# Kernel optimization log

Measured on AMD Instinct MI355X. Metric: run time of the kernel, lower is better.

Reference implementation:

```python
import jax, jax.numpy as jnp
import numpy as np

N = 10000   # num_nodes
E = 320000  # num_edges
D = 256     # feature / hidden dim
H = 256


def adj_lap(edge_index, n):
    """Dense normalized adjacency (gcn_norm, no self loops) and sym Laplacian."""
    row, col = edge_index[0], edge_index[1]
    # dense 0/1 adjacency (duplicate edges overwrite with same value, as in the loop)
    A = jnp.zeros((n, n), dtype=jnp.float32).at[row, col].set(1.0)
    # gcn_norm: deg = scatter(w, col) -> column sums
    deg_c = A.sum(axis=0)
    dinv_c = jnp.where(deg_c > 0, jax.lax.rsqrt(jnp.maximum(deg_c, 1e-12)), 0.0)
    anorm = dinv_c[:, None] * A * dinv_c[None, :]
    # get_laplacian 'sym': deg = scatter(w, row) -> row sums; L = I - D^-1/2 A D^-1/2
    deg_r = A.sum(axis=1)
    dinv_r = jnp.where(deg_r > 0, jax.lax.rsqrt(jnp.maximum(deg_r, 1e-12)), 0.0)
    lap = jnp.eye(n, dtype=jnp.float32) - dinv_r[:, None] * A * dinv_r[None, :]
    return lap, anorm


def gcn2(x, M, W1, b1, W2, b2):
    # pretrain_model: two-layer spectral GCN using propagation matrix M
    h = jax.nn.relu(M @ (x @ W1) + b1)
    return M @ (h @ W2) + b2


def setup_inputs() -> dict:
    key = jax.random.key(0)
    k1, k2, k3, k4 = jax.random.split(key, 4)
    x = jax.random.normal(k1, (N, D), dtype=jnp.float32)
    edge_index = jax.random.randint(k2, (2, E), 0, N, dtype=jnp.int64)
    W1 = jax.random.normal(k3, (D, H), dtype=jnp.float32) * 0.05
    b1 = jnp.zeros((H,), dtype=jnp.float32)
    W2 = jax.random.normal(k4, (H, H), dtype=jnp.float32) * 0.05
    b2 = jnp.zeros((H,), dtype=jnp.float32)
    return {"x": x, "edge_index": edge_index, "W1": W1, "b1": b1, "W2": W2, "b2": b2}


def reference(x, edge_index, W1, b1, W2, b2):
    # identity augmentor: x1 = x2 = x, edge_index1 = edge_index2 = edge_index,
    # so adj_lap is identical for both branches (computed once).
    lsym, anorm = adj_lap(edge_index, x.shape[0])
    z1 = gcn2(x, lsym, W1, b1, W2, b2)   # 'high' pass
    z2 = gcn2(x, anorm, W1, b1, W2, b2)  # 'low' pass
    z = z2
    return (z, z1, z2)
```

## Files before the change

### kernel.cpp

```cpp
#include <hip/hip_runtime.h>

#define NN 10000
#define EE 320000
#define HH 256
#define BKT 192

typedef __attribute__((ext_vector_type(8))) short bf16x8;
typedef __attribute__((ext_vector_type(4))) float f32x4;

__device__ float bf2f(unsigned int v) {
    return __uint_as_float(v << 16);
}
__device__ unsigned short f2bf(float f) {
    unsigned int i = __float_as_uint(f);
    return (unsigned short)((i + 0x7fffu + ((i >> 16) & 1u)) >> 16);
}
__device__ unsigned int fp8e(float f) {
    float a = fabsf(f);
    a = fminf(a, 448.0f);
    unsigned int bits = __float_as_uint(a * __uint_as_float(0x03800000u));
    bits = bits + 0x7ffffu + ((bits >> 20) & 1u);
    unsigned int r = bits >> 20;
    if (r > 0x7eu) r = 0x7eu;
    return r | ((__float_as_uint(f) >> 24) & 0x80u);
}
__device__ float fp8d(unsigned int b) {
    float mag = __uint_as_float((b & 0x7fu) << 20) * __uint_as_float(0x7B800000u);
    return __uint_as_float(((b & 0x80u) << 24) | __float_as_uint(mag));
}
__device__ unsigned int pk2(unsigned short a, unsigned short b) {
    return (unsigned int)a | ((unsigned int)b << 16);
}

__device__ int eload(const void* ei, int is64, int idx) {
    if (is64) return (int)(((const long long*)ei)[idx]);
    return ((const int*)ei)[idx];
}

__global__ void k_init(const unsigned int* xu, const unsigned int* eu, int* flags,
                       int* slotcnt, int* deg_c) {
    int b = blockIdx.x, t = threadIdx.x;
    int i = b * 256 + t;
    if (i < NN) { slotcnt[i] = 0; deg_c[i] = 0; }
    if (b != 0) return;
    __shared__ int odd_nz;
    __shared__ int plaus;
    if (t == 0) { odd_nz = 0; plaus = 0; }
    __syncthreads();
    if (t < 64) {
        for (int k = t; k < 256; k += 64) {
            if (eu[2 * k + 1] != 0) atomicOr(&odd_nz, 1);
        }
        unsigned int lo = xu[t] & 0xffffu;
        unsigned int ex = (lo >> 7) & 0xffu;
        if (lo == 0u || (ex >= 90u && ex <= 150u)) atomicAdd(&plaus, 1);
    }
    __syncthreads();
    if (t == 0) {
        flags[0] = odd_nz ? 0 : 1;
        flags[1] = (plaus >= 56) ? 0 : 1;
    }
}

__global__ void k_prep_scatter(const void* W1, const void* W2, const void* ei,
                               const int* flags, unsigned short* W1sw,
                               unsigned short* W2sw, int* slotcnt,
                               unsigned short* bucket) {
    int b = blockIdx.x;
    if (b >= 64) {
        int e = (b - 64) * 256 + threadIdx.x;
        int is64 = flags[0];
        int r = eload(ei, is64, e);
        int c = eload(ei, is64, EE + e);
        if (r < 0 || r >= NN || c < 0 || c >= NN) return;
        int slot = atomicAdd(&slotcnt[r], 1);
        if (slot < BKT) bucket[(size_t)r * BKT + slot] = (unsigned short)c;
        return;
    }
    const void* W = (b < 32) ? W1 : W2;
    unsigned short* O = (b < 32) ? W1sw : W2sw;
    int g = ((b < 32) ? b : b - 32) * 256 + threadIdx.x;
    int lane = g & 63;
    int n = (g >> 6) & 15;
    int ks = g >> 10;
    int coln = n * 16 + (lane & 15);
    int krow = ks * 32 + ((lane >> 4) & 3) * 8;
    unsigned short v[8];
    if (flags[1]) {
        const float* Wf = (const float*)W;
        #pragma unroll
        for (int j = 0; j < 8; j++) v[j] = f2bf(Wf[(size_t)(krow + j) * HH + coln]);
    } else {
        const unsigned short* Wh = (const unsigned short*)W;
        #pragma unroll
        for (int j = 0; j < 8; j++) v[j] = Wh[(size_t)(krow + j) * HH + coln];
    }
    uint4 p;
    p.x = pk2(v[0], v[1]); p.y = pk2(v[2], v[3]);
    p.z = pk2(v[4], v[5]); p.w = pk2(v[6], v[7]);
    *(uint4*)(O + (size_t)g * 8) = p;
}

__global__ void k_gy_dedup(const void* A, const unsigned short* Bsw,
                           unsigned char* Yf8, void* Oout, const int* flags,
                           const int* slotcnt, unsigned short* bucket,
                           int* deg_r, int* deg_c) {
    __shared__ unsigned short As[16][264];
    __shared__ int lds[4][BKT];
    __shared__ int cnt[4];
    int b = blockIdx.x;
    int tid = threadIdx.x;
    if (b < 625) {
        int r0 = b * 16;
        int af32 = flags[1];
        {
            int row = tid >> 4, seg = tid & 15;
            if (af32) {
                const float* ap = (const float*)A + (size_t)(r0 + row) * HH + seg * 16;
                unsigned short v[16];
                #pragma unroll
                for (int j = 0; j < 16; j += 4) {
                    float4 q = *(const float4*)(ap + j);
                    v[j] = f2bf(q.x); v[j + 1] = f2bf(q.y);
                    v[j + 2] = f2bf(q.z); v[j + 3] = f2bf(q.w);
                }
                uint4 p0, p1;
                p0.x = pk2(v[0], v[1]);  p0.y = pk2(v[2], v[3]);
                p0.z = pk2(v[4], v[5]);  p0.w = pk2(v[6], v[7]);
                p1.x = pk2(v[8], v[9]);  p1.y = pk2(v[10], v[11]);
                p1.z = pk2(v[12], v[13]); p1.w = pk2(v[14], v[15]);
                *(uint4*)&As[row][seg * 16] = p0;
                *(uint4*)&As[row][seg * 16 + 8] = p1;
            } else {
                const unsigned short* ap = (const unsigned short*)A + (size_t)(r0 + row) * HH + seg * 16;
                *(uint4*)&As[row][seg * 16] = *(const uint4*)ap;
                *(uint4*)&As[row][seg * 16 + 8] = *(const uint4*)(ap + 8);
            }
        }
        __syncthreads();
        int wv = tid >> 6;
        int lane = tid & 63;
        int quad = lane >> 4;
        int l16 = lane & 15;
        f32x4 acc[4] = {{0,0,0,0},{0,0,0,0},{0,0,0,0},{0,0,0,0}};
        for (int ks = 0; ks < 8; ks++) {
            bf16x8 af = *(const bf16x8*)&As[l16][ks * 32 + quad * 8];
            #pragma unroll
            for (int t = 0; t < 4; t++) {
                int n = wv * 4 + t;
                bf16x8 bf = *(const bf16x8*)(Bsw + ((size_t)(ks * 16 + n) * 64 + lane) * 8);
                acc[t] = __builtin_amdgcn_mfma_f32_16x16x32_bf16(af, bf, acc[t], 0, 0, 0);
            }
        }
        size_t chunkW = (size_t)NN * HH;
        #pragma unroll
        for (int t = 0; t < 4; t++) {
            int cn = (wv * 4 + t) * 16 + l16;
            #pragma unroll
            for (int r = 0; r < 4; r++) {
                int row = r0 + quad * 4 + r;
                float v = acc[t][r];
                size_t idx = (size_t)row * HH + cn;
                Yf8[idx] = (unsigned char)fp8e(v);
                if (af32) ((float*)Oout)[2 * chunkW + idx] = v;
                else      ((unsigned short*)Oout)[2 * chunkW + idx] = f2bf(v);
            }
        }
        return;
    }
    int wave = tid >> 6;
    int lane = tid & 63;
    int i = (b - 625) * 4 + wave;
    int d = slotcnt[i];
    if (d > BKT) d = BKT;
    if (lane == 0) cnt[wave] = 0;
    unsigned short* bp = bucket + (size_t)i * BKT;
    for (int t = lane; t < d; t += 64) lds[wave][t] = (int)bp[t];
    __syncthreads();
    for (int t = lane; t < d; t += 64) {
        int c = lds[wave][t];
        int dup = 0;
        for (int u = 0; u < t; u++) dup |= (lds[wave][u] == c);
        if (!dup) {
            int p = atomicAdd(&cnt[wave], 1);
            bp[p] = (unsigned short)c;
            atomicAdd(&deg_c[c], 1);
        }
    }
    __syncthreads();
    if (lane == 0) deg_r[i] = cnt[wave];
}

__global__ void k_dinv2(const int* deg_r, const int* deg_c, float* dinv2) {
    int i = blockIdx.x * 256 + threadIdx.x;
    if (i >= NN) return;
    int dr = deg_r[i], dc = deg_c[i];
    dinv2[2 * i]     = dr > 0 ? rsqrtf((float)dr) : 0.0f;
    dinv2[2 * i + 1] = dc > 0 ? rsqrtf((float)dc) : 0.0f;
}

__global__ void k_spmm_mid(const unsigned char* Yf8, const void* Oout,
                           const unsigned short* bucket, const int* ucnt,
                           const float* dinv2, const void* bias,
                           const int* flags, unsigned short* H1, unsigned short* H2) {
    int wave = threadIdx.x >> 6;
    int lane = threadIdx.x & 63;
    int fb = lane * 4;
    int i = blockIdx.x * 4 + wave;
    float a1[4] = {0, 0, 0, 0};
    float a2[4] = {0, 0, 0, 0};
    int n = ucnt[i];
    const unsigned short* cp = bucket + (size_t)i * BKT;
    int t = 0;
    for (; t + 4 <= n; t += 4) {
        ushort4 c4 = *(const ushort4*)(cp + t);
        int cx[4] = {(int)c4.x, (int)c4.y, (int)c4.z, (int)c4.w};
        float2 w[4];
        #pragma unroll
        for (int j = 0; j < 4; j++) w[j] = *(const float2*)(dinv2 + 2 * cx[j]);
        unsigned int gv[4];
        #pragma unroll
        for (int j = 0; j < 4; j++)
            gv[j] = *(const unsigned int*)(Yf8 + (size_t)cx[j] * 256 + fb);
        #pragma unroll
        for (int j = 0; j < 4; j++) {
            #pragma unroll
            for (int k = 0; k < 4; k++) {
                float y = fp8d((gv[j] >> (8 * k)) & 0xffu);
                a1[k] += w[j].x * y;
                a2[k] += w[j].y * y;
            }
        }
    }
    for (; t < n; t++) {
        int c = (int)cp[t];
        float2 w = *(const float2*)(dinv2 + 2 * c);
        unsigned int g = *(const unsigned int*)(Yf8 + (size_t)c * 256 + fb);
        #pragma unroll
        for (int k = 0; k < 4; k++) {
            float y = fp8d((g >> (8 * k)) & 0xffu);
            a1[k] += w.x * y;
            a2[k] += w.y * y;
        }
    }
    int f32io = flags[1];
    float bv[4];
    if (f32io) {
        const float* bp = (const float*)bias + fb;
        #pragma unroll
        for (int k = 0; k < 4; k++) bv[k] = bp[k];
    } else {
        uint2 br = *(const uint2*)((const unsigned short*)bias + fb);
        bv[0] = bf2f(br.x & 0xffffu); bv[1] = bf2f(br.x >> 16);
        bv[2] = bf2f(br.y & 0xffffu); bv[3] = bf2f(br.y >> 16);
    }
    float2 wii = *(const float2*)(dinv2 + 2 * i);
    size_t chunkW = (size_t)NN * HH;
    float yv[4];
    if (f32io) {
        const float* sp = (const float*)Oout + 2 * chunkW + (size_t)i * HH + fb;
        #pragma unroll
        for (int k = 0; k < 4; k++) yv[k] = sp[k];
    } else {
        uint2 yi = *(const uint2*)((const unsigned short*)Oout + 2 * chunkW + (size_t)i * HH + fb);
        yv[0] = bf2f(yi.x & 0xffffu); yv[1] = bf2f(yi.x >> 16);
        yv[2] = bf2f(yi.y & 0xffffu); yv[3] = bf2f(yi.y >> 16);
    }
    float h1[4], h2[4];
    #pragma unroll
    for (int k = 0; k < 4; k++) {
        h1[k] = fmaxf(0.f, yv[k] - wii.x * a1[k] + bv[k]);
        h2[k] = fmaxf(0.f, wii.y * a2[k] + bv[k]);
    }
    uint2 p1, p2;
    p1.x = pk2(f2bf(h1[0]), f2bf(h1[1])); p1.y = pk2(f2bf(h1[2]), f2bf(h1[3]));
    p2.x = pk2(f2bf(h2[0]), f2bf(h2[1])); p2.y = pk2(f2bf(h2[2]), f2bf(h2[3]));
    *(uint2*)(H1 + (size_t)i * HH + fb) = p1;
    *(uint2*)(H2 + (size_t)i * HH + fb) = p2;
}

__global__ void k_gg(const unsigned short* H1, const unsigned short* H2,
                     const unsigned short* Bsw, unsigned char* G12f8,
                     void* Oout, const int* flags) {
    __shared__ unsigned short As[16][264];
    int b = blockIdx.x;
    int tid = threadIdx.x;
    int isG1 = (b < 625);
    const unsigned short* A = isG1 ? H1 : H2;
    int r0 = (isG1 ? b : b - 625) * 16;
    {
        int row = tid >> 4, seg = tid & 15;
        const unsigned short* ap = A + (size_t)(r0 + row) * HH + seg * 16;
        *(uint4*)&As[row][seg * 16] = *(const uint4*)ap;
        *(uint4*)&As[row][seg * 16 + 8] = *(const uint4*)(ap + 8);
    }
    __syncthreads();
    int wv = tid >> 6;
    int lane = tid & 63;
    int quad = lane >> 4;
    int l16 = lane & 15;
    f32x4 acc[4] = {{0,0,0,0},{0,0,0,0},{0,0,0,0},{0,0,0,0}};
    for (int ks = 0; ks < 8; ks++) {
        bf16x8 af = *(const bf16x8*)&As[l16][ks * 32 + quad * 8];
        #pragma unroll
        for (int t = 0; t < 4; t++) {
            int n = wv * 4 + t;
            bf16x8 bf = *(const bf16x8*)(Bsw + ((size_t)(ks * 16 + n) * 64 + lane) * 8);
            acc[t] = __builtin_amdgcn_mfma_f32_16x16x32_bf16(af, bf, acc[t], 0, 0, 0);
        }
    }
    size_t chunkW = (size_t)NN * HH;
    int f32io = flags[1];
    #pragma unroll
    for (int t = 0; t < 4; t++) {
        int cn = (wv * 4 + t) * 16 + l16;
        #pragma unroll
        for (int r = 0; r < 4; r++) {
            int row = r0 + quad * 4 + r;
            float v = acc[t][r];
            if (isG1) {
                G12f8[(size_t)row * 512 + cn] = (unsigned char)fp8e(v);
                size_t idx = (size_t)row * HH + cn;
                if (f32io) ((float*)Oout)[chunkW + idx] = v;
                else       ((unsigned short*)Oout)[chunkW + idx] = f2bf(v);
            } else {
                G12f8[(size_t)row * 512 + 256 + cn] = (unsigned char)fp8e(v);
            }
        }
    }
}

__global__ void k_spmm_fin(const unsigned char* G12f8, const unsigned short* bucket,
                           const int* ucnt, const float* dinv2, const void* bias,
                           const int* flags, void* Oout) {
    int wave = threadIdx.x >> 6;
    int lane = threadIdx.x & 63;
    int half = lane >> 5;
    int sub = lane & 31;
    int fb = sub * 8;
    int goff = half * 256 + fb;
    int i = blockIdx.x * 4 + wave;
    float acc[8] = {0, 0, 0, 0, 0, 0, 0, 0};
    int n = ucnt[i];
    const unsigned short* cp = bucket + (size_t)i * BKT;
    int t = 0;
    for (; t + 4 <= n; t += 4) {
        ushort4 c4 = *(const ushort4*)(cp + t);
        int cx[4] = {(int)c4.x, (int)c4.y, (int)c4.z, (int)c4.w};
        float ws[4];
        #pragma unroll
        for (int j = 0; j < 4; j++) {
            float2 w = *(const float2*)(dinv2 + 2 * cx[j]);
            ws[j] = half ? w.y : w.x;
        }
        uint2 gv[4];
        #pragma unroll
        for (int j = 0; j < 4; j++)
            gv[j] = *(const uint2*)(G12f8 + (size_t)cx[j] * 512 + goff);
        #pragma unroll
        for (int j = 0; j < 4; j++) {
            #pragma unroll
            for (int k = 0; k < 4; k++) {
                float y = fp8d((gv[j].x >> (8 * k)) & 0xffu);
                acc[k] += ws[j] * y;
            }
            #pragma unroll
            for (int k = 0; k < 4; k++) {
                float y = fp8d((gv[j].y >> (8 * k)) & 0xffu);
                acc[4 + k] += ws[j] * y;
            }
        }
    }
    for (; t < n; t++) {
        int c = (int)cp[t];
        float2 w = *(const float2*)(dinv2 + 2 * c);
        float wsel = half ? w.y : w.x;
        uint2 g = *(const uint2*)(G12f8 + (size_t)c * 512 + goff);
        #pragma unroll
        for (int k = 0; k < 4; k++) acc[k] += wsel * fp8d((g.x >> (8 * k)) & 0xffu);
        #pragma unroll
        for (int k = 0; k < 4; k++) acc[4 + k] += wsel * fp8d((g.y >> (8 * k)) & 0xffu);
    }
    int f32io = flags[1];
    float bv[8];
    if (f32io) {
        const float* bp = (const float*)bias + fb;
        #pragma unroll
        for (int k = 0; k < 8; k++) bv[k] = bp[k];
    } else {
        uint4 br = *(const uint4*)((const unsigned short*)bias + fb);
        bv[0] = bf2f(br.x & 0xffffu); bv[1] = bf2f(br.x >> 16);
        bv[2] = bf2f(br.y & 0xffffu); bv[3] = bf2f(br.y >> 16);
        bv[4] = bf2f(br.z & 0xffffu); bv[5] = bf2f(br.z >> 16);
        bv[6] = bf2f(br.w & 0xffffu); bv[7] = bf2f(br.w >> 16);
    }
    float2 wii = *(const float2*)(dinv2 + 2 * i);
    size_t base = (size_t)i * HH + fb;
    size_t chunkW = (size_t)NN * HH;
    float z[8];
    if (half == 0) {
        float gvv[8];
        if (f32io) {
            const float* sp = (const float*)Oout + chunkW + base;
            #pragma unroll
            for (int k = 0; k < 8; k++) gvv[k] = sp[k];
        } else {
            uint4 gi = *(const uint4*)((const unsigned short*)Oout + chunkW + base);
            gvv[0] = bf2f(gi.x & 0xffffu); gvv[1] = bf2f(gi.x >> 16);
            gvv[2] = bf2f(gi.y & 0xffffu); gvv[3] = bf2f(gi.y >> 16);
            gvv[4] = bf2f(gi.z & 0xffffu); gvv[5] = bf2f(gi.z >> 16);
            gvv[6] = bf2f(gi.w & 0xffffu); gvv[7] = bf2f(gi.w >> 16);
        }
        #pragma unroll
        for (int k = 0; k < 8; k++) z[k] = gvv[k] - wii.x * acc[k] + bv[k];
        if (f32io) {
            float* o = (float*)Oout + chunkW + base;
            *(float4*)o = make_float4(z[0], z[1], z[2], z[3]);
            *(float4*)(o + 4) = make_float4(z[4], z[5], z[6], z[7]);
        } else {
            uint4 p;
            p.x = pk2(f2bf(z[0]), f2bf(z[1])); p.y = pk2(f2bf(z[2]), f2bf(z[3]));
            p.z = pk2(f2bf(z[4]), f2bf(z[5])); p.w = pk2(f2bf(z[6]), f2bf(z[7]));
            *(uint4*)((unsigned short*)Oout + chunkW + base) = p;
        }
    } else {
        #pragma unroll
        for (int k = 0; k < 8; k++) z[k] = wii.y * acc[k] + bv[k];
        if (f32io) {
            float* o0 = (float*)Oout + base;
            float* o2 = (float*)Oout + 2 * chunkW + base;
            float4 pa = make_float4(z[0], z[1], z[2], z[3]);
            float4 pb = make_float4(z[4], z[5], z[6], z[7]);
            *(float4*)o0 = pa; *(float4*)(o0 + 4) = pb;
            *(float4*)o2 = pa; *(float4*)(o2 + 4) = pb;
        } else {
            uint4 p;
            p.x = pk2(f2bf(z[0]), f2bf(z[1])); p.y = pk2(f2bf(z[2]), f2bf(z[3]));
            p.z = pk2(f2bf(z[4]), f2bf(z[5])); p.w = pk2(f2bf(z[6]), f2bf(z[7]));
            *(uint4*)((unsigned short*)Oout + base) = p;
            *(uint4*)((unsigned short*)Oout + 2 * chunkW + base) = p;
        }
    }
}

extern "C" void kernel_launch(void* const* d_in, const int* in_sizes, int n_in,
                              void* d_out, int out_size, void* d_ws, size_t ws_size,
                              hipStream_t stream) {
    const void* x = 0; const void* ei = 0;
    const void* W1 = 0; const void* b1 = 0; const void* W2 = 0; const void* b2 = 0;
    for (int i = 0; i < n_in; i++) {
        int s = in_sizes[i];
        if (s == NN * HH) x = d_in[i];
        else if (s == 2 * EE) ei = d_in[i];
        else if (s == HH * HH) { if (!W1) W1 = d_in[i]; else W2 = d_in[i]; }
        else if (s == HH) { if (!b1) b1 = d_in[i]; else b2 = d_in[i]; }
    }

    char* ws = (char*)d_ws;
    size_t off = 0;
    int* flags = (int*)(ws + off); off += 256;
    int* slotcnt = (int*)(ws + off); off += (size_t)NN * 4;
    int* deg_c = (int*)(ws + off); off += (size_t)NN * 4;
    int* deg_r = (int*)(ws + off); off += (size_t)NN * 4;
    float* dinv2 = (float*)(ws + off); off += (size_t)NN * 8;
    unsigned short* bucket = (unsigned short*)(ws + off); off += (size_t)NN * BKT * 2;
    unsigned short* W1sw = (unsigned short*)(ws + off); off += (size_t)HH * HH * 2;
    unsigned short* W2sw = (unsigned short*)(ws + off); off += (size_t)HH * HH * 2;
    unsigned char* Yf8 = (unsigned char*)(ws + off); off += (size_t)NN * 256;
    unsigned char* G12f8 = (unsigned char*)(ws + off); off += (size_t)NN * 512;
    unsigned short* H1 = (unsigned short*)(ws + off); off += (size_t)NN * HH * 2;
    unsigned short* H2 = (unsigned short*)(ws + off); off += (size_t)NN * HH * 2;

    k_init<<<40, 256, 0, stream>>>((const unsigned int*)x, (const unsigned int*)ei,
                                   flags, slotcnt, deg_c);
    k_prep_scatter<<<64 + EE / 256, 256, 0, stream>>>(W1, W2, ei, flags, W1sw, W2sw,
                                                      slotcnt, bucket);
    k_gy_dedup<<<625 + NN / 4, 256, 0, stream>>>(x, W1sw, Yf8, d_out, flags,
                                                 slotcnt, bucket, deg_r, deg_c);
    k_dinv2<<<(NN + 255) / 256, 256, 0, stream>>>(deg_r, deg_c, dinv2);
    k_spmm_mid<<<NN / 4, 256, 0, stream>>>(Yf8, d_out, bucket, deg_r, dinv2, b1,
                                           flags, H1, H2);
    k_gg<<<1250, 256, 0, stream>>>(H1, H2, W2sw, G12f8, d_out, flags);
    k_spmm_fin<<<NN / 4, 256, 0, stream>>>(G12f8, bucket, deg_r, dinv2, b2, flags, d_out);
}
```

Before: 203.3 us.

## Merge all stages into one cooperative persistent kernel with grid syncs

Replaces the seven separate kernel launches with a single cooperative kernel. It loops over virtual blocks and uses grid.sync between stages, which removes per-launch overhead and the separate dinv2 pass. Degree inverses are now recomputed inline with rsqrt from deg_r/deg_c instead of being loaded from a precomputed array. The costs are the grid-wide barrier latency, the occupancy limits that cooperative launch imposes (grid sized from the occupancy query, at most 8 blocks per CU), and extra deg lookups inside the SpMM loops.

```diff
diff --git a/kernel.cpp b/kernel.cpp
--- a/kernel.cpp
+++ b/kernel.cpp
@@ -1,9 +1,13 @@
 #include <hip/hip_runtime.h>
+#include <hip/hip_cooperative_groups.h>
+
+namespace cg = cooperative_groups;
 
 #define NN 10000
 #define EE 320000
 #define HH 256
 #define BKT 192
+#define NTHR 256
 
 typedef __attribute__((ext_vector_type(8))) short bf16x8;
 typedef __attribute__((ext_vector_type(4))) float f32x4;
@@ -31,115 +35,264 @@
 __device__ unsigned int pk2(unsigned short a, unsigned short b) {
     return (unsigned int)a | ((unsigned int)b << 16);
 }
-
 __device__ int eload(const void* ei, int is64, int idx) {
     if (is64) return (int)(((const long long*)ei)[idx]);
     return ((const int*)ei)[idx];
 }
-
-__global__ void k_init(const unsigned int* xu, const unsigned int* eu, int* flags,
-                       int* slotcnt, int* deg_c) {
-    int b = blockIdx.x, t = threadIdx.x;
-    int i = b * 256 + t;
-    if (i < NN) { slotcnt[i] = 0; deg_c[i] = 0; }
-    if (b != 0) return;
-    __shared__ int odd_nz;
-    __shared__ int plaus;
-    if (t == 0) { odd_nz = 0; plaus = 0; }
-    __syncthreads();
-    if (t < 64) {
-        for (int k = t; k < 256; k += 64) {
-            if (eu[2 * k + 1] != 0) atomicOr(&odd_nz, 1);
-        }
-        unsigned int lo = xu[t] & 0xffffu;
-        unsigned int ex = (lo >> 7) & 0xffu;
-        if (lo == 0u || (ex >= 90u && ex <= 150u)) atomicAdd(&plaus, 1);
-    }
-    __syncthreads();
-    if (t == 0) {
-        flags[0] = odd_nz ? 0 : 1;
-        flags[1] = (plaus >= 56) ? 0 : 1;
-    }
-}
-
-__global__ void k_prep_scatter(const void* W1, const void* W2, const void* ei,
-                               const int* flags, unsigned short* W1sw,
-                               unsigned short* W2sw, int* slotcnt,
-                               unsigned short* bucket) {
-    int b = blockIdx.x;
-    if (b >= 64) {
-        int e = (b - 64) * 256 + threadIdx.x;
-        int is64 = flags[0];
-        int r = eload(ei, is64, e);
-        int c = eload(ei, is64, EE + e);
-        if (r < 0 || r >= NN || c < 0 || c >= NN) return;
-        int slot = atomicAdd(&slotcnt[r], 1);
-        if (slot < BKT) bucket[(size_t)r * BKT + slot] = (unsigned short)c;
-        return;
-    }
-    const void* W = (b < 32) ? W1 : W2;
-    unsigned short* O = (b < 32) ? W1sw : W2sw;
-    int g = ((b < 32) ? b : b - 32) * 256 + threadIdx.x;
-    int lane = g & 63;
-    int n = (g >> 6) & 15;
-    int ks = g >> 10;
-    int coln = n * 16 + (lane & 15);
-    int krow = ks * 32 + ((lane >> 4) & 3) * 8;
-    unsigned short v[8];
-    if (flags[1]) {
-        const float* Wf = (const float*)W;
+__device__ __forceinline__ float dinv_of(int d) {
+    return d > 0 ? rsqrtf((float)d) : 0.0f;
+}
+
+__global__ __launch_bounds__(NTHR, 4) void k_mega(
+    const void* x, const void* ei, const void* W1, const void* b1,
+    const void* W2, const void* b2,
+    int* flags, int* slotcnt, int* deg_c, int* deg_r,
+    unsigned short* bucket, unsigned short* W1sw, unsigned short* W2sw,
+    unsigned char* Yf8, unsigned char* G12f8,
+    unsigned short* H1, unsigned short* H2, void* Oout)
+{
+    cg::grid_group grid = cg::this_grid();
+    __shared__ unsigned short As[16][264];
+    __shared__ int dlds[4][BKT];
+    __shared__ int dcnt[4];
+    __shared__ int sh0, sh1;
+    const int tid = threadIdx.x;
+    const int bid = blockIdx.x;
+    const int nb = gridDim.x;
+    const int wave = tid >> 6;
+    const int lane = tid & 63;
+    const size_t chunkW = (size_t)NN * HH;
+
+    if (bid == 0) {
+        if (tid == 0) { sh0 = 0; sh1 = 0; }
+        __syncthreads();
+        if (tid < 64) {
+            const unsigned int* eu = (const unsigned int*)ei;
+            const unsigned int* xu = (const unsigned int*)x;
+            for (int k = tid; k < 256; k += 64)
+                if (eu[2 * k + 1] != 0) atomicOr(&sh0, 1);
+            unsigned int lo = xu[tid] & 0xffffu;
+            unsigned int ex = (lo >> 7) & 0xffu;
+            if (lo == 0u || (ex >= 90u && ex <= 150u)) atomicAdd(&sh1, 1);
+        }
+        __syncthreads();
+        if (tid == 0) {
+            flags[0] = sh0 ? 0 : 1;
+            flags[1] = (sh1 >= 56) ? 0 : 1;
+        }
+    }
+    for (int i = bid * NTHR + tid; i < NN; i += nb * NTHR) {
+        slotcnt[i] = 0;
+        deg_c[i] = 0;
+    }
+    grid.sync();
+
+    const int is64 = flags[0];
+    const int f32io = flags[1];
+
+    for (int vb = bid; vb < 64 + EE / NTHR; vb += nb) {
+        if (vb >= 64) {
+            int e = (vb - 64) * NTHR + tid;
+            int r = eload(ei, is64, e);
+            int c = eload(ei, is64, EE + e);
+            if (r >= 0 && r < NN && c >= 0 && c < NN) {
+                int slot = atomicAdd(&slotcnt[r], 1);
+                if (slot < BKT) bucket[(size_t)r * BKT + slot] = (unsigned short)c;
+            }
+        } else {
+            const void* W = (vb < 32) ? W1 : W2;
+            unsigned short* O = (vb < 32) ? W1sw : W2sw;
+            int g = ((vb < 32) ? vb : vb - 32) * NTHR + tid;
+            int gl = g & 63;
+            int n = (g >> 6) & 15;
+            int ks = g >> 10;
+            int coln = n * 16 + (gl & 15);
+            int krow = ks * 32 + ((gl >> 4) & 3) * 8;
+            unsigned short v[8];
+            if (f32io) {
+                const float* Wf = (const float*)W;
+                #pragma unroll
+                for (int j = 0; j < 8; j++) v[j] = f2bf(Wf[(size_t)(krow + j) * HH + coln]);
+            } else {
+                const unsigned short* Wh = (const unsigned short*)W;
+                #pragma unroll
+                for (int j = 0; j < 8; j++) v[j] = Wh[(size_t)(krow + j) * HH + coln];
+            }
+            uint4 p;
+            p.x = pk2(v[0], v[1]); p.y = pk2(v[2], v[3]);
+            p.z = pk2(v[4], v[5]); p.w = pk2(v[6], v[7]);
+            *(uint4*)(O + (size_t)g * 8) = p;
+        }
+    }
+    grid.sync();
+
+    for (int vb = bid; vb < 625 + NN / 4; vb += nb) {
+        if (vb < 625) {
+            int r0 = vb * 16;
+            __syncthreads();
+            {
+                int row = tid >> 4, seg = tid & 15;
+                if (f32io) {
+                    const float* ap = (const float*)x + (size_t)(r0 + row) * HH + seg * 16;
+                    unsigned short v[16];
+                    #pragma unroll
+                    for (int j = 0; j < 16; j += 4) {
+                        float4 q = *(const float4*)(ap + j);
+                        v[j] = f2bf(q.x); v[j + 1] = f2bf(q.y);
+                        v[j + 2] = f2bf(q.z); v[j + 3] = f2bf(q.w);
+                    }
+                    uint4 p0, p1;
+                    p0.x = pk2(v[0], v[1]);   p0.y = pk2(v[2], v[3]);
+                    p0.z = pk2(v[4], v[5]);   p0.w = pk2(v[6], v[7]);
+                    p1.x = pk2(v[8], v[9]);   p1.y = pk2(v[10], v[11]);
+                    p1.z = pk2(v[12], v[13]); p1.w = pk2(v[14], v[15]);
+                    *(uint4*)&As[row][seg * 16] = p0;
+                    *(uint4*)&As[row][seg * 16 + 8] = p1;
+                } else {
+                    const unsigned short* ap = (const unsigned short*)x + (size_t)(r0 + row) * HH + seg * 16;
+                    *(uint4*)&As[row][seg * 16] = *(const uint4*)ap;
+                    *(uint4*)&As[row][seg * 16 + 8] = *(const uint4*)(ap + 8);
+                }
+            }
+            __syncthreads();
+            int quad = lane >> 4;
+            int l16 = lane & 15;
+            f32x4 acc[4] = {{0,0,0,0},{0,0,0,0},{0,0,0,0},{0,0,0,0}};
+            for (int ks = 0; ks < 8; ks++) {
+                bf16x8 af = *(const bf16x8*)&As[l16][ks * 32 + quad * 8];
+                #pragma unroll
+                for (int t = 0; t < 4; t++) {
+                    int n = wave * 4 + t;
+                    bf16x8 bf = *(const bf16x8*)(W1sw + ((size_t)(ks * 16 + n) * 64 + lane) * 8);
+                    acc[t] = __builtin_amdgcn_mfma_f32_16x16x32_bf16(af, bf, acc[t], 0, 0, 0);
+                }
+            }
+            #pragma unroll
+            for (int t = 0; t < 4; t++) {
+                int cn = (wave * 4 + t) * 16 + l16;
+                #pragma unroll
+                for (int r = 0; r < 4; r++) {
+                    int row = r0 + quad * 4 + r;
+                    float vv = acc[t][r];
+                    size_t idx = (size_t)row * HH + cn;
+                    Yf8[idx] = (unsigned char)fp8e(vv);
+                    if (f32io) ((float*)Oout)[2 * chunkW + idx] = vv;
+                    else       ((unsigned short*)Oout)[2 * chunkW + idx] = f2bf(vv);
+                }
+            }
+        } else {
+            int i = (vb - 625) * 4 + wave;
+            int d = slotcnt[i];
+            if (d > BKT) d = BKT;
+            if (lane == 0) dcnt[wave] = 0;
+            unsigned short* bp = bucket + (size_t)i * BKT;
+            for (int t = lane; t < d; t += 64) dlds[wave][t] = (int)bp[t];
+            for (int t = lane; t < d; t += 64) {
+                int c = dlds[wave][t];
+                int dup = 0;
+                for (int u = 0; u < t; u++) dup |= (dlds[wave][u] == c);
+                if (!dup) {
+                    int p = atomicAdd(&dcnt[wave], 1);
+                    bp[p] = (unsigned short)c;
+                    atomicAdd(&deg_c[c], 1);
+                }
+            }
+            if (lane == 0) deg_r[i] = dcnt[wave];
+        }
+    }
+    grid.sync();
+
+    for (int vb = bid; vb < NN / 4; vb += nb) {
+        int i = vb * 4 + wave;
+        int fb = lane * 4;
+        float a1[4] = {0, 0, 0, 0};
+        float a2[4] = {0, 0, 0, 0};
+        int n = deg_r[i];
+        const unsigned short* cp = bucket + (size_t)i * BKT;
+        int t = 0;
+        for (; t + 4 <= n; t += 4) {
+            ushort4 c4 = *(const ushort4*)(cp + t);
+            int cx[4] = {(int)c4.x, (int)c4.y, (int)c4.z, (int)c4.w};
+            float wx[4], wy[4];
+            #pragma unroll
+            for (int j = 0; j < 4; j++) {
+                wx[j] = dinv_of(deg_r[cx[j]]);
+                wy[j] = dinv_of(deg_c[cx[j]]);
+            }
+            unsigned int gv[4];
+            #pragma unroll
+            for (int j = 0; j < 4; j++)
+                gv[j] = *(const unsigned int*)(Yf8 + (size_t)cx[j] * 256 + fb);
+            #pragma unroll
+            for (int j = 0; j < 4; j++) {
+                #pragma unroll
+                for (int k = 0; k < 4; k++) {
+                    float y = fp8d((gv[j] >> (8 * k)) & 0xffu);
+                    a1[k] += wx[j] * y;
+                    a2[k] += wy[j] * y;
+                }
+            }
+        }
+        for (; t < n; t++) {
+            int c = (int)cp[t];
+            float wx = dinv_of(deg_r[c]);
+            float wy = dinv_of(deg_c[c]);
+            unsigned int g = *(const unsigned int*)(Yf8 + (size_t)c * 256 + fb);
+            #pragma unroll
+            for (int k = 0; k < 4; k++) {
+                float y = fp8d((g >> (8 * k)) & 0xffu);
+                a1[k] += wx * y;
+                a2[k] += wy * y;
+            }
+        }
+        float bv[4];
+        if (f32io) {
+            const float* bp = (const float*)b1 + fb;
+            #pragma unroll
+            for (int k = 0; k < 4; k++) bv[k] = bp[k];
+        } else {
+            uint2 br = *(const uint2*)((const unsigned short*)b1 + fb);
+            bv[0] = bf2f(br.x & 0xffffu); bv[1] = bf2f(br.x >> 16);
+            bv[2] = bf2f(br.y & 0xffffu); bv[3] = bf2f(br.y >> 16);
+        }
+        float wiix = dinv_of(deg_r[i]);
+        float wiiy = dinv_of(deg_c[i]);
+        float yv[4];
+        if (f32io) {
+            const float* sp = (const float*)Oout + 2 * chunkW + (size_t)i * HH + fb;
+            #pragma unroll
+            for (int k = 0; k < 4; k++) yv[k] = sp[k];
+        } else {
+            uint2 yi = *(const uint2*)((const unsigned short*)Oout + 2 * chunkW + (size_t)i * HH + fb);
+            yv[0] = bf2f(yi.x & 0xffffu); yv[1] = bf2f(yi.x >> 16);
+            yv[2] = bf2f(yi.y & 0xffffu); yv[3] = bf2f(yi.y >> 16);
+        }
+        float h1[4], h2[4];
         #pragma unroll
-        for (int j = 0; j < 8; j++) v[j] = f2bf(Wf[(size_t)(krow + j) * HH + coln]);
-    } else {
-        const unsigned short* Wh = (const unsigned short*)W;
-        #pragma unroll
-        for (int j = 0; j < 8; j++) v[j] = Wh[(size_t)(krow + j) * HH + coln];
-    }
-    uint4 p;
-    p.x = pk2(v[0], v[1]); p.y = pk2(v[2], v[3]);
-    p.z = pk2(v[4], v[5]); p.w = pk2(v[6], v[7]);
-    *(uint4*)(O + (size_t)g * 8) = p;
-}
-
-__global__ void k_gy_dedup(const void* A, const unsigned short* Bsw,
-                           unsigned char* Yf8, void* Oout, const int* flags,
-                           const int* slotcnt, unsigned short* bucket,
-                           int* deg_r, int* deg_c) {
-    __shared__ unsigned short As[16][264];
-    __shared__ int lds[4][BKT];
-    __shared__ int cnt[4];
-    int b = blockIdx.x;
-    int tid = threadIdx.x;
-    if (b < 625) {
-        int r0 = b * 16;
-        int af32 = flags[1];
+        for (int k = 0; k < 4; k++) {
+            h1[k] = fmaxf(0.f, yv[k] - wiix * a1[k] + bv[k]);
+            h2[k] = fmaxf(0.f, wiiy * a2[k] + bv[k]);
+        }
+        uint2 p1, p2;
+        p1.x = pk2(f2bf(h1[0]), f2bf(h1[1])); p1.y = pk2(f2bf(h1[2]), f2bf(h1[3]));
+        p2.x = pk2(f2bf(h2[0]), f2bf(h2[1])); p2.y = pk2(f2bf(h2[2]), f2bf(h2[3]));
+        *(uint2*)(H1 + (size_t)i * HH + fb) = p1;
+        *(uint2*)(H2 + (size_t)i * HH + fb) = p2;
+    }
+    grid.sync();
+
+    for (int vb = bid; vb < 1250; vb += nb) {
+        int isG1 = (vb < 625);
+        const unsigned short* A = isG1 ? H1 : H2;
+        int r0 = (isG1 ? vb : vb - 625) * 16;
+        __syncthreads();
         {
             int row = tid >> 4, seg = tid & 15;
-            if (af32) {
-                const float* ap = (const float*)A + (size_t)(r0 + row) * HH + seg * 16;
-                unsigned short v[16];
-                #pragma unroll
-                for (int j = 0; j < 16; j += 4) {
-                    float4 q = *(const float4*)(ap + j);
-                    v[j] = f2bf(q.x); v[j + 1] = f2bf(q.y);
-                    v[j + 2] = f2bf(q.z); v[j + 3] = f2bf(q.w);
-                }
-                uint4 p0, p1;
-                p0.x = pk2(v[0], v[1]);  p0.y = pk2(v[2], v[3]);
-                p0.z = pk2(v[4], v[5]);  p0.w = pk2(v[6], v[7]);
-                p1.x = pk2(v[8], v[9]);  p1.y = pk2(v[10], v[11]);
-                p1.z = pk2(v[12], v[13]); p1.w = pk2(v[14], v[15]);
-                *(uint4*)&As[row][seg * 16] = p0;
-                *(uint4*)&As[row][seg * 16 + 8] = p1;
-            } else {
-                const unsigned short* ap = (const unsigned short*)A + (size_t)(r0 + row) * HH + seg * 16;
-                *(uint4*)&As[row][seg * 16] = *(const uint4*)ap;
-                *(uint4*)&As[row][seg * 16 + 8] = *(const uint4*)(ap + 8);
-            }
+            const unsigned short* ap = A + (size_t)(r0 + row) * HH + seg * 16;
+            *(uint4*)&As[row][seg * 16] = *(const uint4*)ap;
+            *(uint4*)&As[row][seg * 16 + 8] = *(const uint4*)(ap + 8);
         }
         __syncthreads();
-        int wv = tid >> 6;
-        int lane = tid & 63;
         int quad = lane >> 4;
         int l16 = lane & 15;
         f32x4 acc[4] = {{0,0,0,0},{0,0,0,0},{0,0,0,0},{0,0,0,0}};
@@ -147,298 +300,136 @@
             bf16x8 af = *(const bf16x8*)&As[l16][ks * 32 + quad * 8];
             #pragma unroll
             for (int t = 0; t < 4; t++) {
-                int n = wv * 4 + t;
-                bf16x8 bf = *(const bf16x8*)(Bsw + ((size_t)(ks * 16 + n) * 64 + lane) * 8);
+                int n = wave * 4 + t;
+                bf16x8 bf = *(const bf16x8*)(W2sw + ((size_t)(ks * 16 + n) * 64 + lane) * 8);
                 acc[t] = __builtin_amdgcn_mfma_f32_16x16x32_bf16(af, bf, acc[t], 0, 0, 0);
             }
         }
-        size_t chunkW = (size_t)NN * HH;
         #pragma unroll
         for (int t = 0; t < 4; t++) {
-            int cn = (wv * 4 + t) * 16 + l16;
+            int cn = (wave * 4 + t) * 16 + l16;
             #pragma unroll
             for (int r = 0; r < 4; r++) {
                 int row = r0 + quad * 4 + r;
-                float v = acc[t][r];
-                size_t idx = (size_t)row * HH + cn;
-                Yf8[idx] = (unsigned char)fp8e(v);
-                if (af32) ((float*)Oout)[2 * chunkW + idx] = v;
-                else      ((unsigned short*)Oout)[2 * chunkW + idx] = f2bf(v);
-            }
-        }
-        return;
-    }
-    int wave = tid >> 6;
-    int lane = tid & 63;
-    int i = (b - 625) * 4 + wave;
-    int d = slotcnt[i];
-    if (d > BKT) d = BKT;
-    if (lane == 0) cnt[wave] = 0;
-    unsigned short* bp = bucket + (size_t)i * BKT;
-    for (int t = lane; t < d; t += 64) lds[wave][t] = (int)bp[t];
-    __syncthreads();
-    for (int t = lane; t < d; t += 64) {
-        int c = lds[wave][t];
-        int dup = 0;
-        for (int u = 0; u < t; u++) dup |= (lds[wave][u] == c);
-        if (!dup) {
-            int p = atomicAdd(&cnt[wave], 1);
-            bp[p] = (unsigned short)c;
-            atomicAdd(&deg_c[c], 1);
-        }
-    }
-    __syncthreads();
-    if (lane == 0) deg_r[i] = cnt[wave];
-}
-
-__global__ void k_dinv2(const int* deg_r, const int* deg_c, float* dinv2) {
-    int i = blockIdx.x * 256 + threadIdx.x;
-    if (i >= NN) return;
-    int dr = deg_r[i], dc = deg_c[i];
-    dinv2[2 * i]     = dr > 0 ? rsqrtf((float)dr) : 0.0f;
-    dinv2[2 * i + 1] = dc > 0 ? rsqrtf((float)dc) : 0.0f;
-}
-
-__global__ void k_spmm_mid(const unsigned char* Yf8, const void* Oout,
-                           const unsigned short* bucket, const int* ucnt,
-                           const float* dinv2, const void* bias,
-                           const int* flags, unsigned short* H1, unsigned short* H2) {
-    int wave = threadIdx.x >> 6;
-    int lane = threadIdx.x & 63;
-    int fb = lane * 4;
-    int i = blockIdx.x * 4 + wave;
-    float a1[4] = {0, 0, 0, 0};
-    float a2[4] = {0, 0, 0, 0};
-    int n = ucnt[i];
-    const unsigned short* cp = bucket + (size_t)i * BKT;
-    int t = 0;
-    for (; t + 4 <= n; t += 4) {
-        ushort4 c4 = *(const ushort4*)(cp + t);
-        int cx[4] = {(int)c4.x, (int)c4.y, (int)c4.z, (int)c4.w};
-        float2 w[4];
-        #pragma unroll
-        for (int j = 0; j < 4; j++) w[j] = *(const float2*)(dinv2 + 2 * cx[j]);
-        unsigned int gv[4];
-        #pragma unroll
-        for (int j = 0; j < 4; j++)
-            gv[j] = *(const unsigned int*)(Yf8 + (size_t)cx[j] * 256 + fb);
-        #pragma unroll
-        for (int j = 0; j < 4; j++) {
-            #pragma unroll
-            for (int k = 0; k < 4; k++) {
-                float y = fp8d((gv[j] >> (8 * k)) & 0xffu);
-                a1[k] += w[j].x * y;
-                a2[k] += w[j].y * y;
-            }
-        }
-    }
-    for (; t < n; t++) {
-        int c = (int)cp[t];
-        float2 w = *(const float2*)(dinv2 + 2 * c);
-        unsigned int g = *(const unsigned int*)(Yf8 + (size_t)c * 256 + fb);
-        #pragma unroll
-        for (int k = 0; k < 4; k++) {
-            float y = fp8d((g >> (8 * k)) & 0xffu);
-            a1[k] += w.x * y;
-            a2[k] += w.y * y;
-        }
-    }
-    int f32io = flags[1];
-    float bv[4];
-    if (f32io) {
-        const float* bp = (const float*)bias + fb;
-        #pragma unroll
-        for (int k = 0; k < 4; k++) bv[k] = bp[k];
-    } else {
-        uint2 br = *(const uint2*)((const unsigned short*)bias + fb);
-        bv[0] = bf2f(br.x & 0xffffu); bv[1] = bf2f(br.x >> 16);
-        bv[2] = bf2f(br.y & 0xffffu); bv[3] = bf2f(br.y >> 16);
-    }
-    float2 wii = *(const float2*)(dinv2 + 2 * i);
-    size_t chunkW = (size_t)NN * HH;
-    float yv[4];
-    if (f32io) {
-        const float* sp = (const float*)Oout + 2 * chunkW + (size_t)i * HH + fb;
-        #pragma unroll
-        for (int k = 0; k < 4; k++) yv[k] = sp[k];
-    } else {
-        uint2 yi = *(const uint2*)((const unsigned short*)Oout + 2 * chunkW + (size_t)i * HH + fb);
-        yv[0] = bf2f(yi.x & 0xffffu); yv[1] = bf2f(yi.x >> 16);
-        yv[2] = bf2f(yi.y & 0xffffu); yv[3] = bf2f(yi.y >> 16);
-    }
-    float h1[4], h2[4];
-    #pragma unroll
-    for (int k = 0; k < 4; k++) {
-        h1[k] = fmaxf(0.f, yv[k] - wii.x * a1[k] + bv[k]);
-        h2[k] = fmaxf(0.f, wii.y * a2[k] + bv[k]);
-    }
-    uint2 p1, p2;
-    p1.x = pk2(f2bf(h1[0]), f2bf(h1[1])); p1.y = pk2(f2bf(h1[2]), f2bf(h1[3]));
-    p2.x = pk2(f2bf(h2[0]), f2bf(h2[1])); p2.y = pk2(f2bf(h2[2]), f2bf(h2[3]));
-    *(uint2*)(H1 + (size_t)i * HH + fb) = p1;
-    *(uint2*)(H2 + (size_t)i * HH + fb) = p2;
-}
-
-__global__ void k_gg(const unsigned short* H1, const unsigned short* H2,
-                     const unsigned short* Bsw, unsigned char* G12f8,
-                     void* Oout, const int* flags) {
-    __shared__ unsigned short As[16][264];
-    int b = blockIdx.x;
-    int tid = threadIdx.x;
-    int isG1 = (b < 625);
-    const unsigned short* A = isG1 ? H1 : H2;
-    int r0 = (isG1 ? b : b - 625) * 16;
-    {
-        int row = tid >> 4, seg = tid & 15;
-        const unsigned short* ap = A + (size_t)(r0 + row) * HH + seg * 16;
-        *(uint4*)&As[row][seg * 16] = *(const uint4*)ap;
-        *(uint4*)&As[row][seg * 16 + 8] = *(const uint4*)(ap + 8);
-    }
-    __syncthreads();
-    int wv = tid >> 6;
-    int lane = tid & 63;
-    int quad = lane >> 4;
-    int l16 = lane & 15;
-    f32x4 acc[4] = {{0,0,0,0},{0,0,0,0},{0,0,0,0},{0,0,0,0}};
-    for (int ks = 0; ks < 8; ks++) {
-        bf16x8 af = *(const bf16x8*)&As[l16][ks * 32 + quad * 8];
-        #pragma unroll
-        for (int t = 0; t < 4; t++) {
-            int n = wv * 4 + t;
-            bf16x8 bf = *(const bf16x8*)(Bsw + ((size_t)(ks * 16 + n) * 64 + lane) * 8);
-            acc[t] = __builtin_amdgcn_mfma_f32_16x16x32_bf16(af, bf, acc[t], 0, 0, 0);
-        }
-    }
-    size_t chunkW = (size_t)NN * HH;
-    int f32io = flags[1];
-    #pragma unroll
-    for (int t = 0; t < 4; t++) {
-        int cn = (wv * 4 + t) * 16 + l16;
-        #pragma unroll
-        for (int r = 0; r < 4; r++) {
-            int row = r0 + quad * 4 + r;
-            float v = acc[t][r];
-            if (isG1) {
-                G12f8[(size_t)row * 512 + cn] = (unsigned char)fp8e(v);
-                size_t idx = (size_t)row * HH + cn;
-                if (f32io) ((float*)Oout)[chunkW + idx] = v;
-                else       ((unsigned short*)Oout)[chunkW + idx] = f2bf(v);
+                float vv = acc[t][r];
+                if (isG1) {
+                    G12f8[(size_t)row * 512 + cn] = (unsigned char)fp8e(vv);
+                    size_t idx = (size_t)row * HH + cn;
+                    if (f32io) ((float*)Oout)[chunkW + idx] = vv;
+                    else       ((unsigned short*)Oout)[chunkW + idx] = f2bf(vv);
+                } else {
+                    G12f8[(size_t)row * 512 + 256 + cn] = (unsigned char)fp8e(vv);
+                }
+            }
+        }
+    }
+    grid.sync();
+
+    for (int vb = bid; vb < NN / 4; vb += nb) {
+        int half = lane >> 5;
+        int sub = lane & 31;
+        int fb = sub * 8;
+        int goff = half * 256 + fb;
+        int i = vb * 4 + wave;
+        float acc[8] = {0, 0, 0, 0, 0, 0, 0, 0};
+        int n = deg_r[i];
+        const unsigned short* cp = bucket + (size_t)i * BKT;
+        int t = 0;
+        for (; t + 4 <= n; t += 4) {
+            ushort4 c4 = *(const ushort4*)(cp + t);
+            int cx[4] = {(int)c4.x, (int)c4.y, (int)c4.z, (int)c4.w};
+            float ws[4];
+            #pragma unroll
+            for (int j = 0; j < 4; j++) {
+                int dsel = half ? deg_c[cx[j]] : deg_r[cx[j]];
+                ws[j] = dinv_of(dsel);
+            }
+            uint2 gv[4];
+            #pragma unroll
+            for (int j = 0; j < 4; j++)
+                gv[j] = *(const uint2*)(G12f8 + (size_t)cx[j] * 512 + goff);
+            #pragma unroll
+            for (int j = 0; j < 4; j++) {
+                #pragma unroll
+                for (int k = 0; k < 4; k++) {
+                    float y = fp8d((gv[j].x >> (8 * k)) & 0xffu);
+                    acc[k] += ws[j] * y;
+                }
+                #pragma unroll
+                for (int k = 0; k < 4; k++) {
+                    float y = fp8d((gv[j].y >> (8 * k)) & 0xffu);
+                    acc[4 + k] += ws[j] * y;
+                }
+            }
+        }
+        for (; t < n; t++) {
+            int c = (int)cp[t];
+            int dsel = half ? deg_c[c] : deg_r[c];
+            float wsel = dinv_of(dsel);
+            uint2 g = *(const uint2*)(G12f8 + (size_t)c * 512 + goff);
+            #pragma unroll
+            for (int k = 0; k < 4; k++) acc[k] += wsel * fp8d((g.x >> (8 * k)) & 0xffu);
+            #pragma unroll
+            for (int k = 0; k < 4; k++) acc[4 + k] += wsel * fp8d((g.y >> (8 * k)) & 0xffu);
+        }
+        float bv[8];
+        if (f32io) {
+            const float* bp = (const float*)b2 + fb;
+            #pragma unroll
+            for (int k = 0; k < 8; k++) bv[k] = bp[k];
+        } else {
+            uint4 br = *(const uint4*)((const unsigned short*)b2 + fb);
+            bv[0] = bf2f(br.x & 0xffffu); bv[1] = bf2f(br.x >> 16);
+            bv[2] = bf2f(br.y & 0xffffu); bv[3] = bf2f(br.y >> 16);
+            bv[4] = bf2f(br.z & 0xffffu); bv[5] = bf2f(br.z >> 16);
+            bv[6] = bf2f(br.w & 0xffffu); bv[7] = bf2f(br.w >> 16);
+        }
+        size_t base = (size_t)i * HH + fb;
+        float z[8];
+        if (half == 0) {
+            float wiix = dinv_of(deg_r[i]);
+            float gvv[8];
+            if (f32io) {
+                const float* sp = (const float*)Oout + chunkW + base;
+                #pragma unroll
+                for (int k = 0; k < 8; k++) gvv[k] = sp[k];
             } else {
-                G12f8[(size_t)row * 512 + 256 + cn] = (unsigned char)fp8e(v);
-            }
-        }
-    }
-}
-
-__global__ void k_spmm_fin(const unsigned char* G12f8, const unsigned short* bucket,
-                           const int* ucnt, const float* dinv2, const void* bias,
-                           const int* flags, void* Oout) {
-    int wave = threadIdx.x >> 6;
-    int lane = threadIdx.x & 63;
-    int half = lane >> 5;
-    int sub = lane & 31;
-    int fb = sub * 8;
-    int goff = half * 256 + fb;
-    int i = blockIdx.x * 4 + wave;
-    float acc[8] = {0, 0, 0, 0, 0, 0, 0, 0};
-    int n = ucnt[i];
-    const unsigned short* cp = bucket + (size_t)i * BKT;
-    int t = 0;
-    for (; t + 4 <= n; t += 4) {
-        ushort4 c4 = *(const ushort4*)(cp + t);
-        int cx[4] = {(int)c4.x, (int)c4.y, (int)c4.z, (int)c4.w};
-        float ws[4];
-        #pragma unroll
-        for (int j = 0; j < 4; j++) {
-            float2 w = *(const float2*)(dinv2 + 2 * cx[j]);
-            ws[j] = half ? w.y : w.x;
-        }
-        uint2 gv[4];
-        #pragma unroll
-        for (int j = 0; j < 4; j++)
-            gv[j] = *(const uint2*)(G12f8 + (size_t)cx[j] * 512 + goff);
-        #pragma unroll
-        for (int j = 0; j < 4; j++) {
-            #pragma unroll
-            for (int k = 0; k < 4; k++) {
-                float y = fp8d((gv[j].x >> (8 * k)) & 0xffu);
-                acc[k] += ws[j] * y;
-            }
-            #pragma unroll
-            for (int k = 0; k < 4; k++) {
-                float y = fp8d((gv[j].y >> (8 * k)) & 0xffu);
-                acc[4 + k] += ws[j] * y;
-            }
-        }
-    }
-    for (; t < n; t++) {
-        int c = (int)cp[t];
-        float2 w = *(const float2*)(dinv2 + 2 * c);
-        float wsel = half ? w.y : w.x;
-        uint2 g = *(const uint2*)(G12f8 + (size_t)c * 512 + goff);
-        #pragma unroll
-        for (int k = 0; k < 4; k++) acc[k] += wsel * fp8d((g.x >> (8 * k)) & 0xffu);
-        #pragma unroll
-        for (int k = 0; k < 4; k++) acc[4 + k] += wsel * fp8d((g.y >> (8 * k)) & 0xffu);
-    }
-    int f32io = flags[1];
-    float bv[8];
-    if (f32io) {
-        const float* bp = (const float*)bias + fb;
-        #pragma unroll
-        for (int k = 0; k < 8; k++) bv[k] = bp[k];
-    } else {
-        uint4 br = *(const uint4*)((const unsigned short*)bias + fb);
-        bv[0] = bf2f(br.x & 0xffffu); bv[1] = bf2f(br.x >> 16);
-        bv[2] = bf2f(br.y & 0xffffu); bv[3] = bf2f(br.y >> 16);
-        bv[4] = bf2f(br.z & 0xffffu); bv[5] = bf2f(br.z >> 16);
-        bv[6] = bf2f(br.w & 0xffffu); bv[7] = bf2f(br.w >> 16);
-    }
-    float2 wii = *(const float2*)(dinv2 + 2 * i);
-    size_t base = (size_t)i * HH + fb;
-    size_t chunkW = (size_t)NN * HH;
-    float z[8];
-    if (half == 0) {
-        float gvv[8];
-        if (f32io) {
-            const float* sp = (const float*)Oout + chunkW + base;
-            #pragma unroll
-            for (int k = 0; k < 8; k++) gvv[k] = sp[k];
-        } else {
-            uint4 gi = *(const uint4*)((const unsigned short*)Oout + chunkW + base);
-            gvv[0] = bf2f(gi.x & 0xffffu); gvv[1] = bf2f(gi.x >> 16);
-            gvv[2] = bf2f(gi.y & 0xffffu); gvv[3] = bf2f(gi.y >> 16);
-            gvv[4] = bf2f(gi.z & 0xffffu); gvv[5] = bf2f(gi.z >> 16);
-            gvv[6] = bf2f(gi.w & 0xffffu); gvv[7] = bf2f(gi.w >> 16);
-        }
-        #pragma unroll
-        for (int k = 0; k < 8; k++) z[k] = gvv[k] - wii.x * acc[k] + bv[k];
-        if (f32io) {
-            float* o = (float*)Oout + chunkW + base;
-            *(float4*)o = make_float4(z[0], z[1], z[2], z[3]);
-            *(float4*)(o + 4) = make_float4(z[4], z[5], z[6], z[7]);
-        } else {
-            uint4 p;
-            p.x = pk2(f2bf(z[0]), f2bf(z[1])); p.y = pk2(f2bf(z[2]), f2bf(z[3]));
-            p.z = pk2(f2bf(z[4]), f2bf(z[5])); p.w = pk2(f2bf(z[6]), f2bf(z[7]));
-            *(uint4*)((unsigned short*)Oout + chunkW + base) = p;
-        }
-    } else {
-        #pragma unroll
-        for (int k = 0; k < 8; k++) z[k] = wii.y * acc[k] + bv[k];
-        if (f32io) {
-            float* o0 = (float*)Oout + base;
-            float* o2 = (float*)Oout + 2 * chunkW + base;
-            float4 pa = make_float4(z[0], z[1], z[2], z[3]);
-            float4 pb = make_float4(z[4], z[5], z[6], z[7]);
-            *(float4*)o0 = pa; *(float4*)(o0 + 4) = pb;
-            *(float4*)o2 = pa; *(float4*)(o2 + 4) = pb;
-        } else {
-            uint4 p;
-            p.x = pk2(f2bf(z[0]), f2bf(z[1])); p.y = pk2(f2bf(z[2]), f2bf(z[3]));
-            p.z = pk2(f2bf(z[4]), f2bf(z[5])); p.w = pk2(f2bf(z[6]), f2bf(z[7]));
-            *(uint4*)((unsigned short*)Oout + base) = p;
-            *(uint4*)((unsigned short*)Oout + 2 * chunkW + base) = p;
+                uint4 gi = *(const uint4*)((const unsigned short*)Oout + chunkW + base);
+                gvv[0] = bf2f(gi.x & 0xffffu); gvv[1] = bf2f(gi.x >> 16);
+                gvv[2] = bf2f(gi.y & 0xffffu); gvv[3] = bf2f(gi.y >> 16);
+                gvv[4] = bf2f(gi.z & 0xffffu); gvv[5] = bf2f(gi.z >> 16);
+                gvv[6] = bf2f(gi.w & 0xffffu); gvv[7] = bf2f(gi.w >> 16);
+            }
+            #pragma unroll
+            for (int k = 0; k < 8; k++) z[k] = gvv[k] - wiix * acc[k] + bv[k];
+            if (f32io) {
+                float* o = (float*)Oout + chunkW + base;
+                *(float4*)o = make_float4(z[0], z[1], z[2], z[3]);
+                *(float4*)(o + 4) = make_float4(z[4], z[5], z[6], z[7]);
+            } else {
+                uint4 p;
+                p.x = pk2(f2bf(z[0]), f2bf(z[1])); p.y = pk2(f2bf(z[2]), f2bf(z[3]));
+                p.z = pk2(f2bf(z[4]), f2bf(z[5])); p.w = pk2(f2bf(z[6]), f2bf(z[7]));
+                *(uint4*)((unsigned short*)Oout + chunkW + base) = p;
+            }
+        } else {
+            float wiiy = dinv_of(deg_c[i]);
+            #pragma unroll
+            for (int k = 0; k < 8; k++) z[k] = wiiy * acc[k] + bv[k];
+            if (f32io) {
+                float* o0 = (float*)Oout + base;
+                float* o2 = (float*)Oout + 2 * chunkW + base;
+                float4 pa = make_float4(z[0], z[1], z[2], z[3]);
+                float4 pb = make_float4(z[4], z[5], z[6], z[7]);
+                *(float4*)o0 = pa; *(float4*)(o0 + 4) = pb;
+                *(float4*)o2 = pa; *(float4*)(o2 + 4) = pb;
+            } else {
+                uint4 p;
+                p.x = pk2(f2bf(z[0]), f2bf(z[1])); p.y = pk2(f2bf(z[2]), f2bf(z[3]));
+                p.z = pk2(f2bf(z[4]), f2bf(z[5])); p.w = pk2(f2bf(z[6]), f2bf(z[7]));
+                *(uint4*)((unsigned short*)Oout + base) = p;
+                *(uint4*)((unsigned short*)Oout + 2 * chunkW + base) = p;
+            }
         }
     }
 }
@@ -462,7 +453,6 @@
     int* slotcnt = (int*)(ws + off); off += (size_t)NN * 4;
     int* deg_c = (int*)(ws + off); off += (size_t)NN * 4;
     int* deg_r = (int*)(ws + off); off += (size_t)NN * 4;
-    float* dinv2 = (float*)(ws + off); off += (size_t)NN * 8;
     unsigned short* bucket = (unsigned short*)(ws + off); off += (size_t)NN * BKT * 2;
     unsigned short* W1sw = (unsigned short*)(ws + off); off += (size_t)HH * HH * 2;
     unsigned short* W2sw = (unsigned short*)(ws + off); off += (size_t)HH * HH * 2;
@@ -471,15 +461,21 @@
     unsigned short* H1 = (unsigned short*)(ws + off); off += (size_t)NN * HH * 2;
     unsigned short* H2 = (unsigned short*)(ws + off); off += (size_t)NN * HH * 2;
 
-    k_init<<<40, 256, 0, stream>>>((const unsigned int*)x, (const unsigned int*)ei,
-                                   flags, slotcnt, deg_c);
-    k_prep_scatter<<<64 + EE / 256, 256, 0, stream>>>(W1, W2, ei, flags, W1sw, W2sw,
-                                                      slotcnt, bucket);
-    k_gy_dedup<<<625 + NN / 4, 256, 0, stream>>>(x, W1sw, Yf8, d_out, flags,
-                                                 slotcnt, bucket, deg_r, deg_c);
-    k_dinv2<<<(NN + 255) / 256, 256, 0, stream>>>(deg_r, deg_c, dinv2);
-    k_spmm_mid<<<NN / 4, 256, 0, stream>>>(Yf8, d_out, bucket, deg_r, dinv2, b1,
-                                           flags, H1, H2);
-    k_gg<<<1250, 256, 0, stream>>>(H1, H2, W2sw, G12f8, d_out, flags);
-    k_spmm_fin<<<NN / 4, 256, 0, stream>>>(G12f8, bucket, deg_r, dinv2, b2, flags, d_out);
-}
+    static int s_grid = 0;
+    if (s_grid == 0) {
+        int nblk = 0;
+        if (hipOccupancyMaxActiveBlocksPerMultiprocessor(
+                &nblk, (const void*)k_mega, NTHR, 0) != hipSuccess || nblk < 1)
+            nblk = 2;
+        if (nblk > 8) nblk = 8;
+        s_grid = nblk * 256;
+    }
+
+    void* args[] = { (void*)&x, (void*)&ei, (void*)&W1, (void*)&b1, (void*)&W2,
+                     (void*)&b2, (void*)&flags, (void*)&slotcnt, (void*)&deg_c,
+                     (void*)&deg_r, (void*)&bucket, (void*)&W1sw, (void*)&W2sw,
+                     (void*)&Yf8, (void*)&G12f8, (void*)&H1, (void*)&H2,
+                     (void*)&d_out };
+    hipLaunchCooperativeKernel((const void*)k_mega, dim3(s_grid), dim3(NTHR),
+                               args, 0, stream);
+}
```

After: 542.5 us. +166.9%, slower.
